# Kernel optimization log

Measured on AMD Instinct MI355X. Metric: run time of the kernel, lower is better.

The kernel has to match this reference:

```python
import jax, jax.numpy as jnp
import numpy as np

EMBED_DIM = 768
NUM_HEADS = 12
HEAD_DIM = EMBED_DIM // NUM_HEADS
SCALING = HEAD_DIM ** -0.5
B, S = 2, 2048


def setup_inputs() -> dict:
    key = jax.random.key(0)
    k1, k2, k3 = jax.random.split(key, 3)
    x_q = jax.random.normal(k1, (B, S, EMBED_DIM), dtype=jnp.float32)
    # xavier-uniform-ish scaling for weights
    lim_qkv = (6.0 / (EMBED_DIM + 3 * EMBED_DIM)) ** 0.5
    lim_out = (6.0 / (2 * EMBED_DIM)) ** 0.5
    w_qkv = jax.random.uniform(k2, (3 * EMBED_DIM, EMBED_DIM), jnp.float32, -lim_qkv, lim_qkv)
    b_qkv = jnp.zeros((3 * EMBED_DIM,), jnp.float32)
    w_out = jax.random.uniform(k3, (EMBED_DIM, EMBED_DIM), jnp.float32, -lim_out, lim_out)
    b_out = jnp.zeros((EMBED_DIM,), jnp.float32)
    return {"x_q": x_q, "w_qkv": w_qkv, "b_qkv": b_qkv, "w_out": w_out, "b_out": b_out}


def reference(x_q, w_qkv, b_qkv, w_out, b_out):
    b_sz, s_len, _ = x_q.shape
    # qkv projection: (B,S,3E) -> (B,S,3,H,hd) -> split
    qkv = x_q @ w_qkv.T + b_qkv
    qkv = qkv.reshape(b_sz, s_len, 3, NUM_HEADS, HEAD_DIM)
    q = qkv[:, :, 0].transpose(0, 2, 1, 3) * SCALING  # (B,H,S,hd)
    k = qkv[:, :, 1].transpose(0, 2, 1, 3)
    v = qkv[:, :, 2].transpose(0, 2, 1, 3)
    attn = jnp.einsum("bhsd,bhtd->bhst", q, k)  # (B,H,S,S)
    attn = jax.nn.softmax(attn.astype(jnp.float32), axis=-1).astype(attn.dtype)
    out = jnp.einsum("bhst,bhtd->bhsd", attn, v)  # (B,H,S,hd)
    out = out.transpose(0, 2, 1, 3).reshape(b_sz, s_len, EMBED_DIM)
    return out @ w_out.T + b_out
```

## Files before the change

kernel.cpp:

```cpp
#include <hip/hip_runtime.h>
#include <hip/hip_bf16.h>
#include <math.h>

typedef unsigned short u16;
typedef unsigned int u32;
typedef __attribute__((ext_vector_type(8))) short bf16x8;
typedef __attribute__((ext_vector_type(4))) short bf16x4;
typedef __attribute__((ext_vector_type(4))) float f32x4;

#define EMBED 768
#define NHEADS 12
#define HDIM 64
#define NBATCH 2
#define SEQ 2048
#define NTOK 4096
#define QKV_N 2304
#define BHTOT 24
#define QSCALE 0.18033688011112042f

__device__ __forceinline__ u16 f2b(float f) {
    __hip_bfloat16 h = __float2bfloat16(f);
    return __builtin_bit_cast(u16, h);
}
__device__ __forceinline__ u32 pk2(float a, float b) {
    return (u32)f2b(a) | ((u32)f2b(b) << 16);
}
__device__ __forceinline__ f32x4 mfma32(bf16x8 a, bf16x8 b, f32x4 c) {
    return __builtin_amdgcn_mfma_f32_16x16x32_bf16(a, b, c, 0, 0, 0);
}
#if __has_builtin(__builtin_amdgcn_mfma_f32_16x16x16_bf16)
__device__ __forceinline__ f32x4 mfma16(bf16x4 a, bf16x4 b, f32x4 c) {
    return __builtin_amdgcn_mfma_f32_16x16x16_bf16(a, b, c, 0, 0, 0);
}
#else
__device__ __forceinline__ f32x4 mfma16(bf16x4 a, bf16x4 b, f32x4 c) {
    return __builtin_amdgcn_mfma_f32_16x16x16bf16_1k(a, b, c, 0, 0, 0);
}
#endif

#if __has_builtin(__builtin_amdgcn_exp2f)
#define EXP2F __builtin_amdgcn_exp2f
#else
#define EXP2F exp2f
#endif

__device__ __forceinline__ void async16(const u16* g, u16* l) {
    __builtin_amdgcn_global_load_lds(
        (const __attribute__((address_space(1))) unsigned int*)g,
        (__attribute__((address_space(3))) unsigned int*)l,
        16, 0, 0);
}

__global__ __launch_bounds__(256)
void cast_kernel(const float* __restrict__ s0, u16* __restrict__ d0, int n0,
                 const float* __restrict__ s1, u16* __restrict__ d1, int n1,
                 const float* __restrict__ s2, u16* __restrict__ d2, int n2)
{
    int idx = (blockIdx.x * 256 + threadIdx.x) * 4;
    const float* s; u16* d; int i;
    if (idx < n0)            { s = s0; d = d0; i = idx; }
    else if (idx < n0 + n1)  { s = s1; d = d1; i = idx - n0; }
    else                     { s = s2; d = d2; i = idx - n0 - n1; if (i >= n2) return; }
    float4 v = *(const float4*)&s[i];
    ushort4 o;
    o.x = f2b(v.x); o.y = f2b(v.y); o.z = f2b(v.z); o.w = f2b(v.w);
    *(ushort4*)&d[i] = o;
}

__global__ __launch_bounds__(256)
void qkv_gemm(const u16* __restrict__ A, const u16* __restrict__ W,
              const float* __restrict__ bias,
              u16* __restrict__ Qb, u16* __restrict__ Kb, u16* __restrict__ VT)
{
    __shared__ __align__(16) u16 smem[4 * 8192];
    u16* As = smem;
    u16* Bs = smem + 2 * 8192;
    const int m0 = blockIdx.x * 128;
    const int n0 = blockIdx.y * 128;
    const int tid = threadIdx.x;
    const int w = tid >> 6, l = tid & 63;
    const int c = l & 15, q = l >> 4;
    const int wm = (w >> 1) * 64, wn = (w & 1) * 64;
    const int r8 = l >> 3, ch = l & 7;
    const int gch = ch ^ r8;

    #pragma unroll
    for (int j = 0; j < 4; ++j) {
        int row = w * 32 + j * 8 + r8;
        int seg = (w * 32 + j * 8) * 64;
        async16(&A[(size_t)(m0 + row) * EMBED + gch * 8], &As[seg + l * 8]);
        async16(&W[(size_t)(n0 + row) * EMBED + gch * 8], &Bs[seg + l * 8]);
    }

    f32x4 acc[4][4] = {};
    const int NK = EMBED / 64;

    #pragma unroll 2
    for (int kt = 0; kt < NK; ++kt) {
        const int cur = kt & 1;
        __syncthreads();
        if (kt + 1 < NK) {
            int k0 = (kt + 1) * 64;
            #pragma unroll
            for (int j = 0; j < 4; ++j) {
                int row = w * 32 + j * 8 + r8;
                int seg = (cur ^ 1) * 8192 + (w * 32 + j * 8) * 64;
                async16(&A[(size_t)(m0 + row) * EMBED + k0 + gch * 8], &As[seg + l * 8]);
                async16(&W[(size_t)(n0 + row) * EMBED + k0 + gch * 8], &Bs[seg + l * 8]);
            }
        }
        const u16* Ab = As + cur * 8192;
        const u16* Bb = Bs + cur * 8192;
        #pragma unroll
        for (int ks = 0; ks < 2; ++ks) {
            const int cs = (((ks << 2) | q) ^ (c & 7)) << 3;
            bf16x8 af[4], bfr[4];
            #pragma unroll
            for (int i = 0; i < 4; ++i)
                af[i] = *(const bf16x8*)&Ab[(wm + i * 16 + c) * 64 + cs];
            #pragma unroll
            for (int j = 0; j < 4; ++j)
                bfr[j] = *(const bf16x8*)&Bb[(wn + j * 16 + c) * 64 + cs];
            #pragma unroll
            for (int i = 0; i < 4; ++i)
                #pragma unroll
                for (int j = 0; j < 4; ++j)
                    acc[i][j] = mfma32(af[i], bfr[j], acc[i][j]);
        }
    }

    const int p = n0 / EMBED;
    const int ncol0 = n0 + wn;
    const int h = (ncol0 % EMBED) / HDIM;
    const int mrow0 = m0 + wm;
    const int b = mrow0 >> 11;
    const int s0 = mrow0 & (SEQ - 1);

    if (p < 2) {
        u16* dst = (p == 0) ? Qb : Kb;
        const float mul = (p == 0) ? QSCALE : 1.0f;
        #pragma unroll
        for (int j = 0; j < 4; ++j) {
            int n = ncol0 + j * 16 + c;
            int d = j * 16 + c;
            float bval = bias[n];
            #pragma unroll
            for (int i = 0; i < 4; ++i) {
                #pragma unroll
                for (int r = 0; r < 4; ++r) {
                    int s = s0 + i * 16 + q * 4 + r;
                    float v = (acc[i][j][r] + bval) * mul;
                    dst[(((size_t)(b * NHEADS + h)) * SEQ + s) * HDIM + d] = f2b(v);
                }
            }
        }
    } else {
        __syncthreads();
        u16* T = smem + w * (64 * 72);
        #pragma unroll
        for (int j = 0; j < 4; ++j) {
            int n = ncol0 + j * 16 + c;
            float bval = bias[n];
            #pragma unroll
            for (int i = 0; i < 4; ++i) {
                uint2 pr;
                pr.x = pk2(acc[i][j][0] + bval, acc[i][j][1] + bval);
                pr.y = pk2(acc[i][j][2] + bval, acc[i][j][3] + bval);
                *(uint2*)&T[(j * 16 + c) * 72 + i * 16 + q * 4] = pr;
            }
        }
        const size_t vtbase = ((size_t)(b * NHEADS + h)) * HDIM * SEQ + s0;
        #pragma unroll
        for (int ii = 0; ii < 8; ++ii) {
            int d = (l >> 3) + 8 * ii;
            int sch = (l & 7) * 8;
            uint4 vv = *(const uint4*)&T[d * 72 + sch];
            *(uint4*)&VT[vtbase + (size_t)d * SEQ + sch] = vv;
        }
    }
}

__global__ __launch_bounds__(256)
void attn_kernel(const u16* __restrict__ Qb, const u16* __restrict__ Kb,
                 const u16* __restrict__ VT, u16* __restrict__ AO)
{
    __shared__ __align__(16) u16 Ks[3][4096];
    __shared__ __align__(16) u16 Vs[3][4096];

    const int blk = blockIdx.x;
    const int g = blk & 7, kk = blk >> 3;
    const int bh = g * 3 + (kk >> 5);
    const int qt = kk & 31;

    const int tid = threadIdx.x;
    const int w = tid >> 6, l = tid & 63;
    const int c = l & 15, q = l >> 4;

    const u16* qg = Qb + ((size_t)bh * SEQ + qt * 64 + w * 16) * HDIM;
    const u16* kg = Kb + ((size_t)bh * SEQ) * HDIM;
    const u16* vg = VT + ((size_t)bh * HDIM) * SEQ;

    const int r8 = l >> 3, ch = l & 7;
    const int gch = ch ^ r8;

    bf16x8 bq0 = *(const bf16x8*)&qg[c * HDIM + q * 8];
    bf16x8 bq1 = *(const bf16x8*)&qg[c * HDIM + 32 + q * 8];

    f32x4 o[4] = {};
    float lrow = 0.f;

    const int NT = SEQ / 64;

    #pragma unroll
    for (int t0 = 0; t0 < 2; ++t0)
        #pragma unroll
        for (int j = 0; j < 2; ++j) {
            int row = w * 16 + j * 8 + r8;
            int seg = (w * 16 + j * 8) * 64;
            async16(&kg[(size_t)(t0 * 64 + row) * HDIM + gch * 8], &Ks[t0][seg + l * 8]);
            async16(&vg[(size_t)row * SEQ + t0 * 64 + gch * 8],    &Vs[t0][seg + l * 8]);
        }

    int cur = 0, ib = 2;
    for (int kt = 0; kt < NT; ++kt) {
        if (kt + 1 < NT) asm volatile("s_waitcnt vmcnt(4)" ::: "memory");
        else             asm volatile("s_waitcnt vmcnt(0)" ::: "memory");
        __builtin_amdgcn_s_barrier();
        asm volatile("" ::: "memory");

        if (kt + 2 < NT) {
            #pragma unroll
            for (int j = 0; j < 2; ++j) {
                int row = w * 16 + j * 8 + r8;
                int seg = (w * 16 + j * 8) * 64;
                async16(&kg[(size_t)((kt + 2) * 64 + row) * HDIM + gch * 8],
                        &Ks[ib][seg + l * 8]);
                async16(&vg[(size_t)row * SEQ + (kt + 2) * 64 + gch * 8],
                        &Vs[ib][seg + l * 8]);
            }
        }

        const u16* Kss = Ks[cur];
        const u16* Vss = Vs[cur];

        f32x4 sc[4];
        __builtin_amdgcn_s_setprio(1);
        #pragma unroll
        for (int kb = 0; kb < 4; ++kb) {
            bf16x8 ak0 = *(const bf16x8*)&Kss[(kb * 16 + c) * 64 + (((q    ) ^ (c & 7)) << 3)];
            bf16x8 ak1 = *(const bf16x8*)&Kss[(kb * 16 + c) * 64 + (((q | 4) ^ (c & 7)) << 3)];
            f32x4 zz = {};
            zz = mfma32(ak0, bq0, zz);
            sc[kb] = mfma32(ak1, bq1, zz);
        }
        __builtin_amdgcn_s_setprio(0);

        #pragma unroll
        for (int kb = 0; kb < 4; ++kb)
            #pragma unroll
            for (int r = 0; r < 4; ++r) {
                float p = EXP2F(sc[kb][r]);
                sc[kb][r] = p;
                lrow += p;
            }

        bf16x4 bp[4];
        #pragma unroll
        for (int kb = 0; kb < 4; ++kb) {
            uint2 pr;
            pr.x = pk2(sc[kb][0], sc[kb][1]);
            pr.y = pk2(sc[kb][2], sc[kb][3]);
            bp[kb] = __builtin_bit_cast(bf16x4, pr);
        }

        __builtin_amdgcn_s_setprio(1);
        #pragma unroll
        for (int db = 0; db < 4; ++db) {
            bf16x4 av[4];
            #pragma unroll
            for (int kb = 0; kb < 4; ++kb)
                av[kb] = *(const bf16x4*)&Vss[(db * 16 + c) * 64 +
                          (((2 * kb + (q >> 1)) ^ (c & 7)) << 3) + ((q & 1) << 2)];
            f32x4 t = o[db];
            #pragma unroll
            for (int kb = 0; kb < 4; ++kb)
                t = mfma16(av[kb], bp[kb], t);
            o[db] = t;
        }
        __builtin_amdgcn_s_setprio(0);

        cur = (cur == 2) ? 0 : cur + 1;
        ib  = (ib  == 2) ? 0 : ib  + 1;
    }

    lrow += __shfl_xor(lrow, 16);
    lrow += __shfl_xor(lrow, 32);
    float inv = 1.0f / lrow;

    const int b = bh / NHEADS, h = bh % NHEADS;
    const int s = qt * 64 + w * 16 + c;
    u16* ao = AO + ((size_t)(b * SEQ + s)) * EMBED + h * HDIM;
    #pragma unroll
    for (int db = 0; db < 4; ++db) {
        uint2 oo;
        oo.x = pk2(o[db][0] * inv, o[db][1] * inv);
        oo.y = pk2(o[db][2] * inv, o[db][3] * inv);
        *(uint2*)&ao[db * 16 + q * 4] = oo;
    }
}

__global__ __launch_bounds__(256)
void out_gemm(const u16* __restrict__ A, const u16* __restrict__ W,
              const float* __restrict__ bias, float* __restrict__ out)
{
    __shared__ __align__(16) u16 As[2][8192];
    __shared__ __align__(16) u16 Bs[2][4096];
    const int m0 = blockIdx.x * 128;
    const int n0 = blockIdx.y * 64;
    const int tid = threadIdx.x;
    const int w = tid >> 6, l = tid & 63;
    const int c = l & 15, q = l >> 4;
    const int wm = w * 32;
    const int r8 = l >> 3, ch = l & 7;
    const int gch = ch ^ r8;

    #pragma unroll
    for (int j = 0; j < 4; ++j) {
        int row = w * 32 + j * 8 + r8;
        async16(&A[(size_t)(m0 + row) * EMBED + gch * 8],
                &As[0][(w * 32 + j * 8) * 64 + l * 8]);
    }
    #pragma unroll
    for (int j = 0; j < 2; ++j) {
        int row = w * 16 + j * 8 + r8;
        async16(&W[(size_t)(n0 + row) * EMBED + gch * 8],
                &Bs[0][(w * 16 + j * 8) * 64 + l * 8]);
    }

    f32x4 acc[2][4] = {};
    const int NK = EMBED / 64;

    #pragma unroll 2
    for (int kt = 0; kt < NK; ++kt) {
        const int cur = kt & 1;
        __syncthreads();
        if (kt + 1 < NK) {
            int k0 = (kt + 1) * 64;
            #pragma unroll
            for (int j = 0; j < 4; ++j) {
                int row = w * 32 + j * 8 + r8;
                async16(&A[(size_t)(m0 + row) * EMBED + k0 + gch * 8],
                        &As[cur ^ 1][(w * 32 + j * 8) * 64 + l * 8]);
            }
            #pragma unroll
            for (int j = 0; j < 2; ++j) {
                int row = w * 16 + j * 8 + r8;
                async16(&W[(size_t)(n0 + row) * EMBED + k0 + gch * 8],
                        &Bs[cur ^ 1][(w * 16 + j * 8) * 64 + l * 8]);
            }
        }
        #pragma unroll
        for (int ks = 0; ks < 2; ++ks) {
            const int cs = (((ks << 2) | q) ^ (c & 7)) << 3;
            bf16x8 af[2], bfr[4];
            #pragma unroll
            for (int i = 0; i < 2; ++i)
                af[i] = *(const bf16x8*)&As[cur][(wm + i * 16 + c) * 64 + cs];
            #pragma unroll
            for (int j = 0; j < 4; ++j)
                bfr[j] = *(const bf16x8*)&Bs[cur][(j * 16 + c) * 64 + cs];
            #pragma unroll
            for (int i = 0; i < 2; ++i)
                #pragma unroll
                for (int j = 0; j < 4; ++j)
                    acc[i][j] = mfma32(af[i], bfr[j], acc[i][j]);
        }
    }

    #pragma unroll
    for (int j = 0; j < 4; ++j) {
        int n = n0 + j * 16 + c;
        float bval = bias[n];
        #pragma unroll
        for (int i = 0; i < 2; ++i) {
            #pragma unroll
            for (int r = 0; r < 4; ++r) {
                int m = m0 + wm + i * 16 + q * 4 + r;
                out[(size_t)m * EMBED + n] = acc[i][j][r] + bval;
            }
        }
    }
}

extern "C" void kernel_launch(void* const* d_in, const int* in_sizes, int n_in,
                              void* d_out, int out_size, void* d_ws, size_t ws_size,
                              hipStream_t stream)
{
    const float* x    = (const float*)d_in[0];
    const float* wqkv = (const float*)d_in[1];
    const float* bqkv = (const float*)d_in[2];
    const float* wout = (const float*)d_in[3];
    const float* bout = (const float*)d_in[4];
    float* out = (float*)d_out;

    const int nx  = NTOK * EMBED;
    const int nwq = QKV_N * EMBED;
    const int nwo = EMBED * EMBED;
    const size_t per = (size_t)NBATCH * NHEADS * SEQ * HDIM;

    u16* xb    = (u16*)d_ws;
    u16* wqkvb = xb + nx;
    u16* woutb = wqkvb + nwq;
    u16* Qb    = woutb + nwo;
    u16* Kb    = Qb + per;
    u16* VT    = Kb + per;
    u16* AO    = VT + per;

    int castTot = (nx + nwq + nwo) / 4;
    cast_kernel<<<castTot / 256, 256, 0, stream>>>(x, xb, nx, wqkv, wqkvb, nwq, wout, woutb, nwo);

    dim3 g1(NTOK / 128, QKV_N / 128);
    qkv_gemm<<<g1, 256, 0, stream>>>(xb, wqkvb, bqkv, Qb, Kb, VT);

    attn_kernel<<<BHTOT * 32, 256, 0, stream>>>(Qb, Kb, VT, AO);

    dim3 g3(NTOK / 128, EMBED / 64);
    out_gemm<<<g3, 256, 0, stream>>>(AO, woutb, bout, out);
}
```

Measured before the change: 157.6 us.

## Software-pipeline QK^T of next tile with softmax and PV of current tile

Restructures the attention inner loop so each iteration issues the QK^T MFMAs for tile j+1 before doing exp2, packing and the PV MFMAs for tile j. Two score register sets alternate, and the loop is unrolled by six so the triple-buffer indices are compile-time constants. The aim is to hide the exp and pack ALU latency behind independent matrix work and to drop the runtime buffer-index bookkeeping. It also adds a launch-bounds occupancy hint of 3 and routes exp2 through a helper that emits the hardware exp instruction. In exchange, the wait before each iteration becomes vmcnt(0) instead of allowing one tile in flight, which reduces load/compute overlap, and the extra live score registers raise register pressure.

Result: no change. 155.2 us (-1.5%).

```diff
diff --git a/kernel.cpp b/kernel.cpp
--- a/kernel.cpp
+++ b/kernel.cpp
@@ -38,11 +38,15 @@
 }
 #endif
 
+__device__ __forceinline__ float exp2_hw(float x) {
 #if __has_builtin(__builtin_amdgcn_exp2f)
-#define EXP2F __builtin_amdgcn_exp2f
+    return __builtin_amdgcn_exp2f(x);
 #else
-#define EXP2F exp2f
+    float r;
+    asm("v_exp_f32 %0, %1" : "=v"(r) : "v"(x));
+    return r;
 #endif
+}
 
 __device__ __forceinline__ void async16(const u16* g, u16* l) {
     __builtin_amdgcn_global_load_lds(
@@ -180,7 +184,7 @@
     }
 }
 
-__global__ __launch_bounds__(256)
+__global__ __launch_bounds__(256, 3)
 void attn_kernel(const u16* __restrict__ Qb, const u16* __restrict__ Kb,
                  const u16* __restrict__ VT, u16* __restrict__ AO)
 {
@@ -211,87 +215,98 @@
 
     const int NT = SEQ / 64;
 
-    #pragma unroll
-    for (int t0 = 0; t0 < 2; ++t0)
-        #pragma unroll
-        for (int j = 0; j < 2; ++j) {
-            int row = w * 16 + j * 8 + r8;
-            int seg = (w * 16 + j * 8) * 64;
-            async16(&kg[(size_t)(t0 * 64 + row) * HDIM + gch * 8], &Ks[t0][seg + l * 8]);
-            async16(&vg[(size_t)row * SEQ + t0 * 64 + gch * 8],    &Vs[t0][seg + l * 8]);
-        }
-
-    int cur = 0, ib = 2;
-    for (int kt = 0; kt < NT; ++kt) {
-        if (kt + 1 < NT) asm volatile("s_waitcnt vmcnt(4)" ::: "memory");
-        else             asm volatile("s_waitcnt vmcnt(0)" ::: "memory");
-        __builtin_amdgcn_s_barrier();
-        asm volatile("" ::: "memory");
-
-        if (kt + 2 < NT) {
-            #pragma unroll
-            for (int j = 0; j < 2; ++j) {
-                int row = w * 16 + j * 8 + r8;
-                int seg = (w * 16 + j * 8) * 64;
-                async16(&kg[(size_t)((kt + 2) * 64 + row) * HDIM + gch * 8],
-                        &Ks[ib][seg + l * 8]);
-                async16(&vg[(size_t)row * SEQ + (kt + 2) * 64 + gch * 8],
-                        &Vs[ib][seg + l * 8]);
-            }
-        }
-
-        const u16* Kss = Ks[cur];
-        const u16* Vss = Vs[cur];
-
-        f32x4 sc[4];
-        __builtin_amdgcn_s_setprio(1);
-        #pragma unroll
-        for (int kb = 0; kb < 4; ++kb) {
-            bf16x8 ak0 = *(const bf16x8*)&Kss[(kb * 16 + c) * 64 + (((q    ) ^ (c & 7)) << 3)];
-            bf16x8 ak1 = *(const bf16x8*)&Kss[(kb * 16 + c) * 64 + (((q | 4) ^ (c & 7)) << 3)];
-            f32x4 zz = {};
-            zz = mfma32(ak0, bq0, zz);
-            sc[kb] = mfma32(ak1, bq1, zz);
-        }
-        __builtin_amdgcn_s_setprio(0);
-
-        #pragma unroll
-        for (int kb = 0; kb < 4; ++kb)
-            #pragma unroll
-            for (int r = 0; r < 4; ++r) {
-                float p = EXP2F(sc[kb][r]);
-                sc[kb][r] = p;
-                lrow += p;
-            }
-
-        bf16x4 bp[4];
-        #pragma unroll
-        for (int kb = 0; kb < 4; ++kb) {
-            uint2 pr;
-            pr.x = pk2(sc[kb][0], sc[kb][1]);
-            pr.y = pk2(sc[kb][2], sc[kb][3]);
-            bp[kb] = __builtin_bit_cast(bf16x4, pr);
-        }
-
-        __builtin_amdgcn_s_setprio(1);
-        #pragma unroll
-        for (int db = 0; db < 4; ++db) {
-            bf16x4 av[4];
-            #pragma unroll
-            for (int kb = 0; kb < 4; ++kb)
-                av[kb] = *(const bf16x4*)&Vss[(db * 16 + c) * 64 +
-                          (((2 * kb + (q >> 1)) ^ (c & 7)) << 3) + ((q & 1) << 2)];
-            f32x4 t = o[db];
-            #pragma unroll
-            for (int kb = 0; kb < 4; ++kb)
-                t = mfma16(av[kb], bp[kb], t);
-            o[db] = t;
-        }
-        __builtin_amdgcn_s_setprio(0);
-
-        cur = (cur == 2) ? 0 : cur + 1;
-        ib  = (ib  == 2) ? 0 : ib  + 1;
-    }
+#define STAGE(JT, BS) {                                                       \
+    int row0 = w * 16 + r8;                                                   \
+    async16(&kg[(size_t)((JT) * 64 + row0) * HDIM + gch * 8],                 \
+            &Ks[BS][(w * 16) * 64 + l * 8]);                                  \
+    async16(&vg[(size_t)row0 * SEQ + (JT) * 64 + gch * 8],                    \
+            &Vs[BS][(w * 16) * 64 + l * 8]);                                  \
+    async16(&kg[(size_t)((JT) * 64 + row0 + 8) * HDIM + gch * 8],             \
+            &Ks[BS][(w * 16 + 8) * 64 + l * 8]);                              \
+    async16(&vg[(size_t)(row0 + 8) * SEQ + (JT) * 64 + gch * 8],              \
+            &Vs[BS][(w * 16 + 8) * 64 + l * 8]);                              \
+}
+
+#define QKT(SN, BN) {                                                         \
+    __builtin_amdgcn_s_setprio(1);                                            \
+    _Pragma("unroll")                                                         \
+    for (int kb = 0; kb < 4; ++kb) {                                          \
+        bf16x8 ak0 = *(const bf16x8*)&Ks[BN][(kb * 16 + c) * 64 +             \
+                                             (((q    ) ^ (c & 7)) << 3)];     \
+        bf16x8 ak1 = *(const bf16x8*)&Ks[BN][(kb * 16 + c) * 64 +             \
+                                             (((q | 4) ^ (c & 7)) << 3)];     \
+        f32x4 zz = {};                                                        \
+        zz = mfma32(ak0, bq0, zz);                                            \
+        SN[kb] = mfma32(ak1, bq1, zz);                                        \
+    }                                                                         \
+    __builtin_amdgcn_s_setprio(0);                                            \
+}
+
+#define SOFTPV(SC, BC) {                                                      \
+    _Pragma("unroll")                                                         \
+    for (int kb = 0; kb < 4; ++kb) {                                          \
+        float p0 = exp2_hw(SC[kb][0]);                                        \
+        float p1 = exp2_hw(SC[kb][1]);                                        \
+        float p2 = exp2_hw(SC[kb][2]);                                        \
+        float p3 = exp2_hw(SC[kb][3]);                                        \
+        SC[kb][0] = p0; SC[kb][1] = p1; SC[kb][2] = p2; SC[kb][3] = p3;       \
+        lrow += (p0 + p1) + (p2 + p3);                                        \
+    }                                                                         \
+    bf16x4 bp[4];                                                             \
+    _Pragma("unroll")                                                         \
+    for (int kb = 0; kb < 4; ++kb) {                                          \
+        uint2 pr;                                                             \
+        pr.x = pk2(SC[kb][0], SC[kb][1]);                                     \
+        pr.y = pk2(SC[kb][2], SC[kb][3]);                                     \
+        bp[kb] = __builtin_bit_cast(bf16x4, pr);                              \
+    }                                                                         \
+    __builtin_amdgcn_s_setprio(1);                                            \
+    _Pragma("unroll")                                                         \
+    for (int db = 0; db < 4; ++db) {                                          \
+        bf16x4 av[4];                                                         \
+        _Pragma("unroll")                                                     \
+        for (int kb = 0; kb < 4; ++kb)                                        \
+            av[kb] = *(const bf16x4*)&Vs[BC][(db * 16 + c) * 64 +             \
+                      (((2 * kb + (q >> 1)) ^ (c & 7)) << 3) + ((q & 1) << 2)]; \
+        f32x4 t = o[db];                                                      \
+        _Pragma("unroll")                                                     \
+        for (int kb = 0; kb < 4; ++kb) t = mfma16(av[kb], bp[kb], t);         \
+        o[db] = t;                                                            \
+    }                                                                         \
+    __builtin_amdgcn_s_setprio(0);                                            \
+}
+
+#define BODY(J, SC, SN, BC, BN, BS) {                                         \
+    asm volatile("s_waitcnt vmcnt(0)" ::: "memory");                          \
+    __builtin_amdgcn_s_barrier();                                             \
+    if ((J) + 2 < NT) STAGE((J) + 2, BS);                                     \
+    if ((J) + 1 < NT) QKT(SN, BN);                                            \
+    SOFTPV(SC, BC);                                                           \
+}
+
+    f32x4 scA[4], scB[4];
+
+    STAGE(0, 0);
+    STAGE(1, 1);
+    asm volatile("s_waitcnt vmcnt(4)" ::: "memory");
+    __builtin_amdgcn_s_barrier();
+    QKT(scA, 0);
+
+    for (int jb = 0; jb < 30; jb += 6) {
+        BODY(jb + 0, scA, scB, 0, 1, 2);
+        BODY(jb + 1, scB, scA, 1, 2, 0);
+        BODY(jb + 2, scA, scB, 2, 0, 1);
+        BODY(jb + 3, scB, scA, 0, 1, 2);
+        BODY(jb + 4, scA, scB, 1, 2, 0);
+        BODY(jb + 5, scB, scA, 2, 0, 1);
+    }
+    BODY(30, scA, scB, 0, 1, 2);
+    SOFTPV(scB, 1);
+
+#undef STAGE
+#undef QKT
+#undef SOFTPV
+#undef BODY
 
     lrow += __shfl_xor(lrow, 16);
     lrow += __shfl_xor(lrow, 32);
```

## Split attention KV across wave pairs, load V directly to registers

Applied to the files above, without the earlier changes.

The attention kernel now processes 32 query rows per block instead of 64, launches twice as many blocks, and has pairs of waves split each 64-key tile so each wave handles 32 keys. The partial outputs and row sums from the two waves are combined through shared memory at the end. V is loaded straight from global memory into registers in the MFMA operand layout rather than staged in LDS, which drops the V shared buffers and raises the occupancy hint. The aim is more parallelism and occupancy with fewer LDS reads, at the cost of each block re-reading K and V for fewer queries, uncoalesced 8-byte V loads, and an extra reduction step.

After: 296.9 us. 1.88x slower.

```diff
diff --git a/kernel.cpp b/kernel.cpp
--- a/kernel.cpp
+++ b/kernel.cpp
@@ -38,11 +38,15 @@
 }
 #endif
 
+__device__ __forceinline__ float exp2_hw(float x) {
 #if __has_builtin(__builtin_amdgcn_exp2f)
-#define EXP2F __builtin_amdgcn_exp2f
+    return __builtin_amdgcn_exp2f(x);
 #else
-#define EXP2F exp2f
+    float r;
+    asm("v_exp_f32 %0, %1" : "=v"(r) : "v"(x));
+    return r;
 #endif
+}
 
 __device__ __forceinline__ void async16(const u16* g, u16* l) {
     __builtin_amdgcn_global_load_lds(
@@ -180,25 +184,25 @@
     }
 }
 
-__global__ __launch_bounds__(256)
+__global__ __launch_bounds__(256, 5)
 void attn_kernel(const u16* __restrict__ Qb, const u16* __restrict__ Kb,
                  const u16* __restrict__ VT, u16* __restrict__ AO)
 {
     __shared__ __align__(16) u16 Ks[3][4096];
-    __shared__ __align__(16) u16 Vs[3][4096];
 
     const int blk = blockIdx.x;
     const int g = blk & 7, kk = blk >> 3;
-    const int bh = g * 3 + (kk >> 5);
-    const int qt = kk & 31;
+    const int bh = g * 3 + (kk >> 6);
+    const int qt = kk & 63;
 
     const int tid = threadIdx.x;
     const int w = tid >> 6, l = tid & 63;
     const int c = l & 15, q = l >> 4;
-
-    const u16* qg = Qb + ((size_t)bh * SEQ + qt * 64 + w * 16) * HDIM;
+    const int wq = w >> 1, wk = w & 1;
+
+    const u16* qg = Qb + ((size_t)bh * SEQ + qt * 32 + wq * 16) * HDIM;
     const u16* kg = Kb + ((size_t)bh * SEQ) * HDIM;
-    const u16* vg = VT + ((size_t)bh * HDIM) * SEQ;
+    const u16* vg = VT + ((size_t)bh * HDIM) * SEQ + wk * 32 + q * 4;
 
     const int r8 = l >> 3, ch = l & 7;
     const int gch = ch ^ r8;
@@ -211,101 +215,109 @@
 
     const int NT = SEQ / 64;
 
-    #pragma unroll
-    for (int t0 = 0; t0 < 2; ++t0)
-        #pragma unroll
-        for (int j = 0; j < 2; ++j) {
-            int row = w * 16 + j * 8 + r8;
-            int seg = (w * 16 + j * 8) * 64;
-            async16(&kg[(size_t)(t0 * 64 + row) * HDIM + gch * 8], &Ks[t0][seg + l * 8]);
-            async16(&vg[(size_t)row * SEQ + t0 * 64 + gch * 8],    &Vs[t0][seg + l * 8]);
-        }
-
-    int cur = 0, ib = 2;
-    for (int kt = 0; kt < NT; ++kt) {
-        if (kt + 1 < NT) asm volatile("s_waitcnt vmcnt(4)" ::: "memory");
-        else             asm volatile("s_waitcnt vmcnt(0)" ::: "memory");
+    {
+        int row0 = w * 16 + r8;
+        async16(&kg[(size_t)(row0     ) * HDIM + gch * 8], &Ks[0][(w * 16    ) * 64 + l * 8]);
+        async16(&kg[(size_t)(row0 +  8) * HDIM + gch * 8], &Ks[0][(w * 16 + 8) * 64 + l * 8]);
+        async16(&kg[(size_t)(64 + row0    ) * HDIM + gch * 8], &Ks[1][(w * 16    ) * 64 + l * 8]);
+        async16(&kg[(size_t)(64 + row0 + 8) * HDIM + gch * 8], &Ks[1][(w * 16 + 8) * 64 + l * 8]);
+    }
+
+    const u16* kbase = &Ks[0][0];
+    int sR = 0, sW = 2;
+
+    for (int j = 0; j < NT; ++j) {
+        uint2 vr[4][2];
+        #pragma unroll
+        for (int db = 0; db < 4; ++db)
+            #pragma unroll
+            for (int kb2 = 0; kb2 < 2; ++kb2)
+                vr[db][kb2] = *(const uint2*)&vg[(size_t)(db * 16 + c) * SEQ + j * 64 + kb2 * 16];
+
+        asm volatile("s_waitcnt vmcnt(10)" ::: "memory");
         __builtin_amdgcn_s_barrier();
-        asm volatile("" ::: "memory");
-
-        if (kt + 2 < NT) {
-            #pragma unroll
-            for (int j = 0; j < 2; ++j) {
-                int row = w * 16 + j * 8 + r8;
-                int seg = (w * 16 + j * 8) * 64;
-                async16(&kg[(size_t)((kt + 2) * 64 + row) * HDIM + gch * 8],
-                        &Ks[ib][seg + l * 8]);
-                async16(&vg[(size_t)row * SEQ + (kt + 2) * 64 + gch * 8],
-                        &Vs[ib][seg + l * 8]);
-            }
-        }
-
-        const u16* Kss = Ks[cur];
-        const u16* Vss = Vs[cur];
-
-        f32x4 sc[4];
+
+        if (j + 2 < NT) {
+            int row0 = w * 16 + r8;
+            u16* kst = (u16*)kbase + sW * 4096;
+            async16(&kg[(size_t)((j + 2) * 64 + row0     ) * HDIM + gch * 8],
+                    &kst[(w * 16    ) * 64 + l * 8]);
+            async16(&kg[(size_t)((j + 2) * 64 + row0 +  8) * HDIM + gch * 8],
+                    &kst[(w * 16 + 8) * 64 + l * 8]);
+        }
+
+        const u16* kr = kbase + sR * 4096;
+        f32x4 sc[2];
         __builtin_amdgcn_s_setprio(1);
         #pragma unroll
-        for (int kb = 0; kb < 4; ++kb) {
-            bf16x8 ak0 = *(const bf16x8*)&Kss[(kb * 16 + c) * 64 + (((q    ) ^ (c & 7)) << 3)];
-            bf16x8 ak1 = *(const bf16x8*)&Kss[(kb * 16 + c) * 64 + (((q | 4) ^ (c & 7)) << 3)];
+        for (int kb2 = 0; kb2 < 2; ++kb2) {
+            bf16x8 ak0 = *(const bf16x8*)&kr[(wk * 32 + kb2 * 16 + c) * 64 +
+                                             (((q    ) ^ (c & 7)) << 3)];
+            bf16x8 ak1 = *(const bf16x8*)&kr[(wk * 32 + kb2 * 16 + c) * 64 +
+                                             (((q | 4) ^ (c & 7)) << 3)];
             f32x4 zz = {};
             zz = mfma32(ak0, bq0, zz);
-            sc[kb] = mfma32(ak1, bq1, zz);
+            sc[kb2] = mfma32(ak1, bq1, zz);
         }
         __builtin_amdgcn_s_setprio(0);
 
-        #pragma unroll
-        for (int kb = 0; kb < 4; ++kb)
-            #pragma unroll
-            for (int r = 0; r < 4; ++r) {
-                float p = EXP2F(sc[kb][r]);
-                sc[kb][r] = p;
-                lrow += p;
-            }
-
-        bf16x4 bp[4];
-        #pragma unroll
-        for (int kb = 0; kb < 4; ++kb) {
+        bf16x4 bp[2];
+        #pragma unroll
+        for (int kb2 = 0; kb2 < 2; ++kb2) {
+            float p0 = exp2_hw(sc[kb2][0]);
+            float p1 = exp2_hw(sc[kb2][1]);
+            float p2 = exp2_hw(sc[kb2][2]);
+            float p3 = exp2_hw(sc[kb2][3]);
+            lrow += (p0 + p1) + (p2 + p3);
             uint2 pr;
-            pr.x = pk2(sc[kb][0], sc[kb][1]);
-            pr.y = pk2(sc[kb][2], sc[kb][3]);
-            bp[kb] = __builtin_bit_cast(bf16x4, pr);
+            pr.x = pk2(p0, p1);
+            pr.y = pk2(p2, p3);
+            bp[kb2] = __builtin_bit_cast(bf16x4, pr);
         }
 
         __builtin_amdgcn_s_setprio(1);
         #pragma unroll
         for (int db = 0; db < 4; ++db) {
-            bf16x4 av[4];
-            #pragma unroll
-            for (int kb = 0; kb < 4; ++kb)
-                av[kb] = *(const bf16x4*)&Vss[(db * 16 + c) * 64 +
-                          (((2 * kb + (q >> 1)) ^ (c & 7)) << 3) + ((q & 1) << 2)];
             f32x4 t = o[db];
-            #pragma unroll
-            for (int kb = 0; kb < 4; ++kb)
-                t = mfma16(av[kb], bp[kb], t);
+            t = mfma16(__builtin_bit_cast(bf16x4, vr[db][0]), bp[0], t);
+            t = mfma16(__builtin_bit_cast(bf16x4, vr[db][1]), bp[1], t);
             o[db] = t;
         }
         __builtin_amdgcn_s_setprio(0);
 
-        cur = (cur == 2) ? 0 : cur + 1;
-        ib  = (ib  == 2) ? 0 : ib  + 1;
+        sR = (sR == 2) ? 0 : sR + 1;
+        sW = (sW == 2) ? 0 : sW + 1;
     }
 
     lrow += __shfl_xor(lrow, 16);
     lrow += __shfl_xor(lrow, 32);
-    float inv = 1.0f / lrow;
-
-    const int b = bh / NHEADS, h = bh % NHEADS;
-    const int s = qt * 64 + w * 16 + c;
-    u16* ao = AO + ((size_t)(b * SEQ + s)) * EMBED + h * HDIM;
-    #pragma unroll
-    for (int db = 0; db < 4; ++db) {
-        uint2 oo;
-        oo.x = pk2(o[db][0] * inv, o[db][1] * inv);
-        oo.y = pk2(o[db][2] * inv, o[db][3] * inv);
-        *(uint2*)&ao[db * 16 + q * 4] = oo;
+
+    __syncthreads();
+    float* SCR = (float*)&Ks[0][0];
+    float* LR  = SCR + 2048;
+
+    if (wk == 1) {
+        #pragma unroll
+        for (int db = 0; db < 4; ++db)
+            *(f32x4*)&SCR[((wq * 4 + db) << 8) + l * 4] = o[db];
+        if (q == 0) LR[wq * 16 + c] = lrow;
+    }
+    __syncthreads();
+
+    if (wk == 0) {
+        float inv = 1.0f / (lrow + LR[wq * 16 + c]);
+        const int b = bh / NHEADS, h = bh % NHEADS;
+        const int s = qt * 32 + wq * 16 + c;
+        u16* ao = AO + ((size_t)(b * SEQ + s)) * EMBED + h * HDIM;
+        #pragma unroll
+        for (int db = 0; db < 4; ++db) {
+            f32x4 part = *(const f32x4*)&SCR[((wq * 4 + db) << 8) + l * 4];
+            f32x4 t = o[db] + part;
+            uint2 oo;
+            oo.x = pk2(t[0] * inv, t[1] * inv);
+            oo.y = pk2(t[2] * inv, t[3] * inv);
+            *(uint2*)&ao[db * 16 + q * 4] = oo;
+        }
     }
 }
 
@@ -422,7 +434,7 @@
     dim3 g1(NTOK / 128, QKV_N / 128);
     qkv_gemm<<<g1, 256, 0, stream>>>(xb, wqkvb, bqkv, Qb, Kb, VT);
 
-    attn_kernel<<<BHTOT * 32, 256, 0, stream>>>(Qb, Kb, VT, AO);
+    attn_kernel<<<BHTOT * 64, 256, 0, stream>>>(Qb, Kb, VT, AO);
 
     dim3 g3(NTOK / 128, EMBED / 64);
     out_gemm<<<g3, 256, 0, stream>>>(AO, woutb, bout, out);
```
